# Kernel optimization log

Measured on AMD Instinct MI355X. Metric: run time of the kernel, lower is better.

## Reference

```python
import jax, jax.numpy as jnp
import numpy as np

D_IN, D_K, D_V, BLOCK = 1024, 64, 64, 2048
B, T = 4, 2048

def setup_inputs() -> dict:
    key = jax.random.key(0)
    k0, k1, k2, k3 = jax.random.split(key, 4)
    x = jax.random.normal(k0, (B, T, D_IN), dtype=jnp.float32)
    s = 1.0 / np.sqrt(D_IN)
    Wq = jax.random.normal(k1, (D_IN, D_K), dtype=jnp.float32) * s
    Wk = jax.random.normal(k2, (D_IN, D_K), dtype=jnp.float32) * s
    Wv = jax.random.normal(k3, (D_IN, D_V), dtype=jnp.float32) * s
    return {"x": x, "Wq": Wq, "Wk": Wk, "Wv": Wv}

def reference(x, Wq, Wk, Wv):
    # Q,K,V projections (Linear without bias)
    Q = jnp.einsum('btc,ck->btk', x, Wq)
    K = jnp.einsum('btc,ck->btk', x, Wk)
    V = jnp.einsum('btc,cv->btv', x, Wv)
    Tq = x.shape[1]
    scores = jnp.einsum('bqk,btk->bqt', Q, K)  # [B,T,T]
    causal = jnp.tril(jnp.ones((Tq, Tq), dtype=bool))
    scores = jnp.where(causal, scores, -jnp.inf)
    attn = jax.nn.softmax(scores, axis=-1)
    # NOTE: original divides the AV product by sqrt(d_k) AFTER softmax
    out = jnp.einsum('bqt,btv->bqv', attn, V) / jnp.sqrt(jnp.asarray(K.shape[-1], dtype=x.dtype))
    return out
```

## Files before the change

kernel.cpp:

```cpp
#include <hip/hip_runtime.h>
#include <math.h>

typedef unsigned short u16;
typedef unsigned int uint32;
typedef __attribute__((ext_vector_type(4))) float f32x4;
typedef __attribute__((ext_vector_type(4))) unsigned int u32x4;
typedef __bf16 bf16x8 __attribute__((ext_vector_type(8)));

#define MFMA16(a,b,c) __builtin_amdgcn_mfma_f32_16x16x32_bf16((a),(b),(c),0,0,0)

typedef const __attribute__((address_space(1))) unsigned GU;
typedef __attribute__((address_space(3))) unsigned LU;
__device__ __forceinline__ void gl_lds16(const void* g, void* l) {
    __builtin_amdgcn_global_load_lds((GU*)g, (LU*)l, 16, 0, 0);
}

__device__ __forceinline__ u16 f2b(float f) {
    __bf16 h = (__bf16)f;
    return __builtin_bit_cast(u16, h);
}
__device__ __forceinline__ float b2f(u16 u) {
    unsigned v = (unsigned)u << 16;
    return __builtin_bit_cast(float, v);
}

__device__ __forceinline__ void agload4(f32x4& d, const float* p) {
    asm volatile("global_load_dwordx4 %0, %1, off" : "=&v"(d) : "v"(p) : "memory");
}
__device__ __forceinline__ void dsr(bf16x8& d, uint32 a) {
    u32x4 tmp;
    asm volatile("ds_read_b128 %0, %1" : "=&v"(tmp) : "v"(a) : "memory");
    d = __builtin_bit_cast(bf16x8, tmp);
}
#define WAITVM_I(n) asm volatile("s_waitcnt vmcnt(" #n ")" ::: "memory")
#define WAITVM(n) WAITVM_I(n)

__global__ __launch_bounds__(128) void wtrans_kernel(
    const float* __restrict__ Wq, const float* __restrict__ Wk,
    const float* __restrict__ Wv, u16* __restrict__ Wt2)
{
    const int n = blockIdx.x;
    const float* W = (n < 64) ? Wq : ((n < 128) ? Wk : Wv);
    const int nc = n & 63, cg = n >> 4, r = n & 15;
    const int t = threadIdx.x;
    const int k0 = t * 8;
    const int kstep = k0 >> 6, kh = (k0 >> 5) & 1, kg = (k0 >> 3) & 3;
    u16 hh[8], ll[8];
#pragma unroll
    for (int i = 0; i < 8; ++i) {
        const float a = W[(size_t)(k0 + i) * 64 + nc];
        hh[i] = f2b(a);
        ll[i] = f2b(a - b2f(hh[i]));
    }
    const size_t fi = (size_t)kstep * 48 + (size_t)cg * 4 + (size_t)kh * 2;
    u16* dst = Wt2 + fi * 512 + kg * 128 + r * 8;
    uint4 vh, vl;
    vh.x = (uint)hh[0] | ((uint)hh[1] << 16); vh.y = (uint)hh[2] | ((uint)hh[3] << 16);
    vh.z = (uint)hh[4] | ((uint)hh[5] << 16); vh.w = (uint)hh[6] | ((uint)hh[7] << 16);
    vl.x = (uint)ll[0] | ((uint)ll[1] << 16); vl.y = (uint)ll[2] | ((uint)ll[3] << 16);
    vl.z = (uint)ll[4] | ((uint)ll[5] << 16); vl.w = (uint)ll[6] | ((uint)ll[7] << 16);
    *(uint4*)dst         = vh;
    *(uint4*)(dst + 512) = vl;
}

__global__ __launch_bounds__(512) void proj_kernel(
    const float* __restrict__ x, const u16* __restrict__ Wt2,
    u16* __restrict__ Qhi, u16* __restrict__ Qlo,
    u16* __restrict__ Khi, u16* __restrict__ Klo, u16* __restrict__ Vt)
{
    __shared__ u16 WB[3][48][512];
    __shared__ u16 vs[32][72];

    const int t = threadIdx.x, w = t >> 6, lane = t & 63;
    const int lo = lane & 15, hi = lane >> 4;
    const int mh = w & 1, nt = w >> 1;
    const int row0 = blockIdx.x * 32;

    f32x4 acc[3];
#pragma unroll
    for (int i = 0; i < 3; ++i) acc[i] = (f32x4){0.f, 0.f, 0.f, 0.f};

    const float* xrow = x + (size_t)(row0 + mh * 16 + lo) * 1024 + hi * 8;
    const uint32 ldsbase = (uint32)(size_t)(LU*)(&WB[0][0][0]);

    f32x4 xr[3][4];

    auto stageS = [&](int buf, int s) {
#pragma unroll
        for (int i = 0; i < 6; ++i)
            gl_lds16(Wt2 + ((size_t)s * 48 + w * 6 + i) * 512 + lane * 8,
                     &WB[buf][w * 6 + i][0]);
    };
    auto issueX = [&](f32x4 (&xv)[4], int s) {
#pragma unroll
        for (int kh = 0; kh < 2; ++kh)
#pragma unroll
            for (int j = 0; j < 2; ++j)
                agload4(xv[kh * 2 + j], xrow + s * 64 + kh * 32 + j * 4);
    };
    auto computeS = [&](int buf, const f32x4 (&xv)[4]) {
        bf16x8 wf[12];
        const uint32 bb = ldsbase + (uint32)buf * 49152u
                        + (uint32)(nt * 12) * 1024u + (uint32)lane * 16u;
#pragma unroll
        for (int j = 0; j < 12; ++j)
            dsr(wf[j], bb + (uint32)j * 1024u);
        asm volatile("s_waitcnt lgkmcnt(0)" ::: "memory");
        __builtin_amdgcn_sched_barrier(0);
        __builtin_amdgcn_s_setprio(1);
#pragma unroll
        for (int kh = 0; kh < 2; ++kh) {
            bf16x8 ah, al;
#pragma unroll
            for (int e = 0; e < 4; ++e) {
                { float v = xv[kh * 2][e];     __bf16 hb = (__bf16)v; ah[e] = hb;     al[e] = (__bf16)(v - (float)hb); }
                { float v = xv[kh * 2 + 1][e]; __bf16 hb = (__bf16)v; ah[4 + e] = hb; al[4 + e] = (__bf16)(v - (float)hb); }
            }
#pragma unroll
            for (int i = 0; i < 3; ++i) {
                const bf16x8 wh = wf[i * 4 + kh * 2 + 0];
                const bf16x8 wl = wf[i * 4 + kh * 2 + 1];
                acc[i] = MFMA16(ah, wh, acc[i]);
                acc[i] = MFMA16(ah, wl, acc[i]);
                acc[i] = MFMA16(al, wh, acc[i]);
            }
        }
        __builtin_amdgcn_s_setprio(0);
    };

    stageS(0, 0);
    issueX(xr[0], 0);
    stageS(1, 1);
    issueX(xr[1], 1);

#define PSTEP(S_, N1_)                                                  \
    do {                                                                \
        WAITVM(N1_);                                                    \
        __builtin_amdgcn_sched_barrier(0);                              \
        __builtin_amdgcn_s_barrier();                                   \
        __builtin_amdgcn_sched_barrier(0);                              \
        if ((S_) + 2 <= 15) {                                           \
            stageS(((S_) + 2) % 3, (S_) + 2);                           \
            issueX(xr[((S_) + 2) % 3], (S_) + 2);                       \
        }                                                               \
        computeS((S_) % 3, xr[(S_) % 3]);                               \
    } while (0)

    PSTEP(0, 10);  PSTEP(1, 10);  PSTEP(2, 10);  PSTEP(3, 10);
    PSTEP(4, 10);  PSTEP(5, 10);  PSTEP(6, 10);  PSTEP(7, 10);
    PSTEP(8, 10);  PSTEP(9, 10);  PSTEP(10, 10); PSTEP(11, 10);
    PSTEP(12, 10); PSTEP(13, 10); PSTEP(14, 10); PSTEP(15, 0);
#undef PSTEP

#pragma unroll
    for (int i = 0; i < 3; ++i) {
        const int cg = nt * 3 + i;
#pragma unroll
        for (int r = 0; r < 4; ++r) {
            const float v = acc[i][r];
            const int row = row0 + mh * 16 + hi * 4 + r;
            const u16 h = f2b(v);
            if (cg < 4) {
                Qhi[(size_t)row * 64 + cg * 16 + lo] = h;
                Qlo[(size_t)row * 64 + cg * 16 + lo] = f2b(v - b2f(h));
            } else if (cg < 8) {
                Khi[(size_t)row * 64 + (cg - 4) * 16 + lo] = h;
                Klo[(size_t)row * 64 + (cg - 4) * 16 + lo] = f2b(v - b2f(h));
            } else {
                vs[mh * 16 + hi * 4 + r][(cg - 8) * 16 + lo] = h;
            }
        }
    }
    __syncthreads();
    {
        const int bb = row0 >> 11, tok0 = row0 & 2047;
        const int d = t >> 3, part = t & 7;
        u16 tmp[4];
#pragma unroll
        for (int i = 0; i < 4; ++i) tmp[i] = vs[part * 4 + i][d];
        uint2 v2;
        v2.x = (uint)tmp[0] | ((uint)tmp[1] << 16);
        v2.y = (uint)tmp[2] | ((uint)tmp[3] << 16);
        *(uint2*)(Vt + (size_t)bb * 131072 + (size_t)d * 2048 + tok0 + part * 4) = v2;
    }
}

__global__ __launch_bounds__(512, 2) void attn_kernel(
    const u16* __restrict__ Qhi, const u16* __restrict__ Qlo,
    const u16* __restrict__ Khi, const u16* __restrict__ Klo,
    const u16* __restrict__ Vt, float* __restrict__ out)
{
    __shared__ u16 P[8][16 * 64];
    __shared__ float OA[8][16][64];
    __shared__ float LS[8][16];

    const int pi = blockIdx.x, b = blockIdx.y;
    const int t = threadIdx.x, w = t >> 6, l = t & 63;
    const int lo = l & 15, hi = l >> 4;

    const u16* Qh = Qhi + (size_t)b * 131072;
    const u16* Ql = Qlo + (size_t)b * 131072;
    const u16* Kh = Khi + (size_t)b * 131072;
    const u16* Kl = Klo + (size_t)b * 131072;
    const u16* V  = Vt  + (size_t)b * 131072;

    u16* Pw = P[w];

#pragma unroll 1
    for (int phase = 0; phase < 2; ++phase) {
        const int p = phase ? pi : (127 - pi);
        const int q0 = p * 16;
        const int nt = (p >> 2) + 1;

        bf16x8 aqh[2], aql[2];
#pragma unroll
        for (int s = 0; s < 2; ++s) {
            aqh[s] = *(const bf16x8*)(Qh + (size_t)(q0 + lo) * 64 + s * 32 + hi * 8);
            aql[s] = *(const bf16x8*)(Ql + (size_t)(q0 + lo) * 64 + s * 32 + hi * 8);
        }

        f32x4 acc[4];
        float ls[4];
#pragma unroll
        for (int r = 0; r < 4; ++r) { acc[r] = (f32x4){0.f,0.f,0.f,0.f}; ls[r] = 0.f; }

        bf16x8 kh[4][2], kl[4][2];
        auto loadK = [&](int j0) {
#pragma unroll
            for (int kg = 0; kg < 4; ++kg)
#pragma unroll
                for (int s = 0; s < 2; ++s) {
                    const size_t off = (size_t)(j0 + kg * 16 + lo) * 64 + s * 32 + hi * 8;
                    kh[kg][s] = *(const bf16x8*)(Kh + off);
                    kl[kg][s] = *(const bf16x8*)(Kl + off);
                }
        };

        if (w < nt) loadK(w * 64);
#pragma unroll 1
        for (int j = w; j < nt; j += 8) {
            const int j0 = j * 64;
            bf16x8 bv[4][2];
#pragma unroll
            for (int dg = 0; dg < 4; ++dg)
#pragma unroll
                for (int s = 0; s < 2; ++s)
                    bv[dg][s] = *(const bf16x8*)(V + (size_t)(dg * 16 + lo) * 2048 + j0 + s * 32 + hi * 8);

            f32x4 S[4];
            const f32x4 zf = (f32x4){0.f,0.f,0.f,0.f};
            __builtin_amdgcn_s_setprio(1);
#pragma unroll
            for (int kg = 0; kg < 4; ++kg) {
                f32x4 sv = zf;
                sv = MFMA16(aqh[0], kh[kg][0], sv);
                sv = MFMA16(aqh[1], kh[kg][1], sv);
                sv = MFMA16(aqh[0], kl[kg][0], sv);
                sv = MFMA16(aqh[1], kl[kg][1], sv);
                sv = MFMA16(aql[0], kh[kg][0], sv);
                sv = MFMA16(aql[1], kh[kg][1], sv);
                S[kg] = sv;
            }
            __builtin_amdgcn_s_setprio(0);

            if (j + 8 < nt) loadK((j + 8) * 64);

            const bool dm = (j == nt - 1);
#pragma unroll
            for (int r = 0; r < 4; ++r) {
                const int row = q0 + hi * 4 + r;
                float sv0 = S[0][r], sv1 = S[1][r], sv2 = S[2][r], sv3 = S[3][r];
                if (dm) {
                    sv0 = (j0 +      lo > row) ? -INFINITY : sv0;
                    sv1 = (j0 + 16 + lo > row) ? -INFINITY : sv1;
                    sv2 = (j0 + 32 + lo > row) ? -INFINITY : sv2;
                    sv3 = (j0 + 48 + lo > row) ? -INFINITY : sv3;
                }
                const u16 u0 = f2b(__expf(sv0)), u1 = f2b(__expf(sv1));
                const u16 u2 = f2b(__expf(sv2)), u3 = f2b(__expf(sv3));
                ls[r] += (b2f(u0) + b2f(u1)) + (b2f(u2) + b2f(u3));
                const int rowL = hi * 4 + r;
                const int base = rowL * 64;
                const int sw = rowL & 7;
                Pw[base + (((0 + (lo >> 3)) ^ sw) << 3) + (lo & 7)] = u0;
                Pw[base + (((2 + (lo >> 3)) ^ sw) << 3) + (lo & 7)] = u1;
                Pw[base + (((4 + (lo >> 3)) ^ sw) << 3) + (lo & 7)] = u2;
                Pw[base + (((6 + (lo >> 3)) ^ sw) << 3) + (lo & 7)] = u3;
            }
            const bf16x8 pa0 = *(const bf16x8*)&Pw[lo * 64 + (((hi    ) ^ (lo & 7)) << 3)];
            const bf16x8 pa1 = *(const bf16x8*)&Pw[lo * 64 + (((hi + 4) ^ (lo & 7)) << 3)];
            __builtin_amdgcn_s_setprio(1);
#pragma unroll
            for (int dg = 0; dg < 4; ++dg) {
                acc[dg] = MFMA16(pa0, bv[dg][0], acc[dg]);
                acc[dg] = MFMA16(pa1, bv[dg][1], acc[dg]);
            }
            __builtin_amdgcn_s_setprio(0);
        }

#pragma unroll
        for (int r = 0; r < 4; ++r) {
#pragma unroll
            for (int msk = 8; msk; msk >>= 1) ls[r] += __shfl_xor(ls[r], msk, 64);
        }

#pragma unroll
        for (int r = 0; r < 4; ++r) {
            if (lo == 0) LS[w][hi * 4 + r] = ls[r];
#pragma unroll
            for (int dg = 0; dg < 4; ++dg) OA[w][hi * 4 + r][dg * 16 + lo] = acc[dg][r];
        }
        __syncthreads();

        {
            const int row = t >> 5, c0 = (t & 31) * 2;
            float s0 = 0.f, s1 = 0.f, Lt = 0.f;
#pragma unroll
            for (int wv = 0; wv < 8; ++wv) {
                s0 += OA[wv][row][c0];
                s1 += OA[wv][row][c0 + 1];
                Lt += LS[wv][row];
            }
            const float inv = 0.125f / Lt;
            float2 o = make_float2(s0 * inv, s1 * inv);
            *(float2*)(out + ((size_t)b * 2048 + q0 + row) * 64 + c0) = o;
        }
        __syncthreads();
    }
}

extern "C" void kernel_launch(void* const* d_in, const int* in_sizes, int n_in,
                              void* d_out, int out_size, void* d_ws, size_t ws_size,
                              hipStream_t stream) {
    const float* x  = (const float*)d_in[0];
    const float* Wq = (const float*)d_in[1];
    const float* Wk = (const float*)d_in[2];
    const float* Wv = (const float*)d_in[3];
    float* outp = (float*)d_out;

    u16* Wt2 = (u16*)d_ws;
    u16* Qhi = Wt2 + 393216;
    u16* Qlo = Qhi + 524288;
    u16* Khi = Qlo + 524288;
    u16* Klo = Khi + 524288;
    u16* Vt  = Klo + 524288;

    wtrans_kernel<<<dim3(192), dim3(128), 0, stream>>>(Wq, Wk, Wv, Wt2);
    proj_kernel<<<dim3(256), dim3(512), 0, stream>>>(x, Wt2, Qhi, Qlo, Khi, Klo, Vt);
    attn_kernel<<<dim3(64, 4), dim3(512), 0, stream>>>(Qhi, Qlo, Khi, Klo, Vt, outp);
}
```

Before: 61.51 us.

## Split attention key range across two blocks and add combine kernel; halve projection stage

The attention kernel now launches twice as many blocks. Each block handles half of the key tiles for a query tile and writes unnormalized partial outputs and row sums to workspace. A new combine kernel adds the two halves and applies the normalization. The projection kernel's pipeline stage is halved to 32 columns of K per step, which gives 32 stages with a smaller LDS footprint and fewer registers. The aim is more parallelism and occupancy, paid for with an extra launch and extra global traffic for the partials.

```diff
diff --git a/kernel.cpp b/kernel.cpp
--- a/kernel.cpp
+++ b/kernel.cpp
@@ -68,7 +68,7 @@
     u16* __restrict__ Qhi, u16* __restrict__ Qlo,
     u16* __restrict__ Khi, u16* __restrict__ Klo, u16* __restrict__ Vt)
 {
-    __shared__ u16 WB[3][48][512];
+    __shared__ u16 WB[3][24][512];
     __shared__ u16 vs[32][72];
 
     const int t = threadIdx.x, w = t >> 6, lane = t & 63;
@@ -83,47 +83,44 @@
     const float* xrow = x + (size_t)(row0 + mh * 16 + lo) * 1024 + hi * 8;
     const uint32 ldsbase = (uint32)(size_t)(LU*)(&WB[0][0][0]);
 
-    f32x4 xr[3][4];
+    f32x4 xr[3][2];
 
     auto stageS = [&](int buf, int s) {
 #pragma unroll
-        for (int i = 0; i < 6; ++i)
-            gl_lds16(Wt2 + ((size_t)s * 48 + w * 6 + i) * 512 + lane * 8,
-                     &WB[buf][w * 6 + i][0]);
+        for (int i = 0; i < 3; ++i) {
+            const int j = w * 3 + i;
+            const int cg = j >> 1, hl = j & 1;
+            const size_t fi = (size_t)(s >> 1) * 48 + (size_t)cg * 4 + (size_t)(s & 1) * 2 + hl;
+            gl_lds16(Wt2 + fi * 512 + lane * 8, &WB[buf][j][0]);
+        }
     };
-    auto issueX = [&](f32x4 (&xv)[4], int s) {
-#pragma unroll
-        for (int kh = 0; kh < 2; ++kh)
-#pragma unroll
-            for (int j = 0; j < 2; ++j)
-                agload4(xv[kh * 2 + j], xrow + s * 64 + kh * 32 + j * 4);
+    auto issueX = [&](f32x4 (&xv)[2], int s) {
+        agload4(xv[0], xrow + s * 32);
+        agload4(xv[1], xrow + s * 32 + 4);
     };
-    auto computeS = [&](int buf, const f32x4 (&xv)[4]) {
-        bf16x8 wf[12];
-        const uint32 bb = ldsbase + (uint32)buf * 49152u
-                        + (uint32)(nt * 12) * 1024u + (uint32)lane * 16u;
-#pragma unroll
-        for (int j = 0; j < 12; ++j)
-            dsr(wf[j], bb + (uint32)j * 1024u);
+    auto computeS = [&](int buf, const f32x4 (&xv)[2]) {
+        bf16x8 wf[6];
+        const uint32 bb = ldsbase + (uint32)buf * 24576u + (uint32)lane * 16u;
+#pragma unroll
+        for (int i = 0; i < 3; ++i) {
+            const int cg = nt * 3 + i;
+            dsr(wf[i * 2 + 0], bb + (uint32)(cg * 2 + 0) * 1024u);
+            dsr(wf[i * 2 + 1], bb + (uint32)(cg * 2 + 1) * 1024u);
+        }
         asm volatile("s_waitcnt lgkmcnt(0)" ::: "memory");
         __builtin_amdgcn_sched_barrier(0);
+        bf16x8 ah, al;
+#pragma unroll
+        for (int e = 0; e < 4; ++e) {
+            { float v = xv[0][e]; __bf16 hb = (__bf16)v; ah[e] = hb;     al[e] = (__bf16)(v - (float)hb); }
+            { float v = xv[1][e]; __bf16 hb = (__bf16)v; ah[4 + e] = hb; al[4 + e] = (__bf16)(v - (float)hb); }
+        }
         __builtin_amdgcn_s_setprio(1);
 #pragma unroll
-        for (int kh = 0; kh < 2; ++kh) {
-            bf16x8 ah, al;
-#pragma unroll
-            for (int e = 0; e < 4; ++e) {
-                { float v = xv[kh * 2][e];     __bf16 hb = (__bf16)v; ah[e] = hb;     al[e] = (__bf16)(v - (float)hb); }
-                { float v = xv[kh * 2 + 1][e]; __bf16 hb = (__bf16)v; ah[4 + e] = hb; al[4 + e] = (__bf16)(v - (float)hb); }
-            }
-#pragma unroll
-            for (int i = 0; i < 3; ++i) {
-                const bf16x8 wh = wf[i * 4 + kh * 2 + 0];
-                const bf16x8 wl = wf[i * 4 + kh * 2 + 1];
-                acc[i] = MFMA16(ah, wh, acc[i]);
-                acc[i] = MFMA16(ah, wl, acc[i]);
-                acc[i] = MFMA16(al, wh, acc[i]);
-            }
+        for (int i = 0; i < 3; ++i) {
+            acc[i] = MFMA16(ah, wf[i * 2 + 0], acc[i]);
+            acc[i] = MFMA16(ah, wf[i * 2 + 1], acc[i]);
+            acc[i] = MFMA16(al, wf[i * 2 + 0], acc[i]);
         }
         __builtin_amdgcn_s_setprio(0);
     };
@@ -139,17 +136,21 @@
         __builtin_amdgcn_sched_barrier(0);                              \
         __builtin_amdgcn_s_barrier();                                   \
         __builtin_amdgcn_sched_barrier(0);                              \
-        if ((S_) + 2 <= 15) {                                           \
+        if ((S_) + 2 <= 31) {                                           \
             stageS(((S_) + 2) % 3, (S_) + 2);                           \
             issueX(xr[((S_) + 2) % 3], (S_) + 2);                       \
         }                                                               \
         computeS((S_) % 3, xr[(S_) % 3]);                               \
     } while (0)
 
-    PSTEP(0, 10);  PSTEP(1, 10);  PSTEP(2, 10);  PSTEP(3, 10);
-    PSTEP(4, 10);  PSTEP(5, 10);  PSTEP(6, 10);  PSTEP(7, 10);
-    PSTEP(8, 10);  PSTEP(9, 10);  PSTEP(10, 10); PSTEP(11, 10);
-    PSTEP(12, 10); PSTEP(13, 10); PSTEP(14, 10); PSTEP(15, 0);
+    PSTEP(0, 5);  PSTEP(1, 5);  PSTEP(2, 5);  PSTEP(3, 5);
+    PSTEP(4, 5);  PSTEP(5, 5);  PSTEP(6, 5);  PSTEP(7, 5);
+    PSTEP(8, 5);  PSTEP(9, 5);  PSTEP(10, 5); PSTEP(11, 5);
+    PSTEP(12, 5); PSTEP(13, 5); PSTEP(14, 5); PSTEP(15, 5);
+    PSTEP(16, 5); PSTEP(17, 5); PSTEP(18, 5); PSTEP(19, 5);
+    PSTEP(20, 5); PSTEP(21, 5); PSTEP(22, 5); PSTEP(23, 5);
+    PSTEP(24, 5); PSTEP(25, 5); PSTEP(26, 5); PSTEP(27, 5);
+    PSTEP(28, 5); PSTEP(29, 5); PSTEP(30, 5); PSTEP(31, 0);
 #undef PSTEP
 
 #pragma unroll
@@ -188,15 +189,17 @@
 __global__ __launch_bounds__(512, 2) void attn_kernel(
     const u16* __restrict__ Qhi, const u16* __restrict__ Qlo,
     const u16* __restrict__ Khi, const u16* __restrict__ Klo,
-    const u16* __restrict__ Vt, float* __restrict__ out)
+    const u16* __restrict__ Vt, float* __restrict__ OP, float* __restrict__ LSP)
 {
     __shared__ u16 P[8][16 * 64];
     __shared__ float OA[8][16][64];
     __shared__ float LS[8][16];
 
-    const int pi = blockIdx.x, b = blockIdx.y;
+    const int bx = blockIdx.x, b = blockIdx.y;
+    const int pi = bx >> 1, h = bx & 1;
     const int t = threadIdx.x, w = t >> 6, l = t & 63;
     const int lo = l & 15, hi = l >> 4;
+    const int sw0 = h * 8 + w;
 
     const u16* Qh = Qhi + (size_t)b * 131072;
     const u16* Ql = Qlo + (size_t)b * 131072;
@@ -236,9 +239,9 @@
                 }
         };
 
-        if (w < nt) loadK(w * 64);
+        if (sw0 < nt) loadK(sw0 * 64);
 #pragma unroll 1
-        for (int j = w; j < nt; j += 8) {
+        for (int j = sw0; j < nt; j += 16) {
             const int j0 = j * 64;
             bf16x8 bv[4][2];
 #pragma unroll
@@ -263,7 +266,7 @@
             }
             __builtin_amdgcn_s_setprio(0);
 
-            if (j + 8 < nt) loadK((j + 8) * 64);
+            if (j + 16 < nt) loadK((j + 16) * 64);
 
             const bool dm = (j == nt - 1);
 #pragma unroll
@@ -321,12 +324,28 @@
                 s1 += OA[wv][row][c0 + 1];
                 Lt += LS[wv][row];
             }
-            const float inv = 0.125f / Lt;
-            float2 o = make_float2(s0 * inv, s1 * inv);
-            *(float2*)(out + ((size_t)b * 2048 + q0 + row) * 64 + c0) = o;
+            const size_t gofs = (size_t)h * 524288 + ((size_t)b * 2048 + q0 + row) * 64 + c0;
+            *(float2*)(OP + gofs) = make_float2(s0, s1);
+            if ((t & 31) == 0) LSP[(size_t)h * 8192 + (size_t)b * 2048 + q0 + row] = Lt;
         }
         __syncthreads();
     }
+}
+
+__global__ __launch_bounds__(256) void combine_kernel(
+    const float* __restrict__ OP, const float* __restrict__ LSP, float* __restrict__ out)
+{
+    const int i4 = blockIdx.x * 256 + threadIdx.x;
+    const int row = i4 >> 4;
+    const int c = (i4 & 15) * 4;
+    const float4 a0 = *(const float4*)(OP + ((size_t)row << 6) + c);
+    const float4 a1 = *(const float4*)(OP + 524288 + ((size_t)row << 6) + c);
+    const float Lt = LSP[row] + LSP[8192 + row];
+    const float inv = 0.125f / Lt;
+    float4 o;
+    o.x = (a0.x + a1.x) * inv; o.y = (a0.y + a1.y) * inv;
+    o.z = (a0.z + a1.z) * inv; o.w = (a0.w + a1.w) * inv;
+    *(float4*)(out + ((size_t)row << 6) + c) = o;
 }
 
 extern "C" void kernel_launch(void* const* d_in, const int* in_sizes, int n_in,
@@ -344,8 +363,11 @@
     u16* Khi = Qlo + 524288;
     u16* Klo = Khi + 524288;
     u16* Vt  = Klo + 524288;
+    float* OP  = (float*)(Vt + 524288);
+    float* LSP = OP + 1048576;
 
     wtrans_kernel<<<dim3(192), dim3(128), 0, stream>>>(Wq, Wk, Wv, Wt2);
     proj_kernel<<<dim3(256), dim3(512), 0, stream>>>(x, Wt2, Qhi, Qlo, Khi, Klo, Vt);
-    attn_kernel<<<dim3(64, 4), dim3(512), 0, stream>>>(Qhi, Qlo, Khi, Klo, Vt, outp);
-}
+    attn_kernel<<<dim3(128, 4), dim3(512), 0, stream>>>(Qhi, Qlo, Khi, Klo, Vt, OP, LSP);
+    combine_kernel<<<dim3(512), dim3(256), 0, stream>>>(OP, LSP, outp);
+}
```

New measurement: 76.27 us. 1.24x slower.

## Split projection K-dimension across waves and reduce partial sums via LDS

Applied to the files above, without the earlier changes.

Each wave now handles both 16-row halves but only half of each 64-wide K step, instead of one row half over the full K step. Each wave therefore reads only 6 weight fragments per step instead of 12, so each weight fragment is reused across two row tiles and LDS read traffic drops. The cost is an extra LDS reduction at the end, which adds two barriers. The x global loads are also reorganized per row half.

```diff
diff --git a/kernel.cpp b/kernel.cpp
--- a/kernel.cpp
+++ b/kernel.cpp
@@ -73,56 +73,62 @@
 
     const int t = threadIdx.x, w = t >> 6, lane = t & 63;
     const int lo = lane & 15, hi = lane >> 4;
-    const int mh = w & 1, nt = w >> 1;
+    const int kq = w & 1, nt = w >> 1;
     const int row0 = blockIdx.x * 32;
 
-    f32x4 acc[3];
-#pragma unroll
-    for (int i = 0; i < 3; ++i) acc[i] = (f32x4){0.f, 0.f, 0.f, 0.f};
-
-    const float* xrow = x + (size_t)(row0 + mh * 16 + lo) * 1024 + hi * 8;
+    f32x4 acc[2][3];
+#pragma unroll
+    for (int rh = 0; rh < 2; ++rh)
+#pragma unroll
+        for (int i = 0; i < 3; ++i) acc[rh][i] = (f32x4){0.f, 0.f, 0.f, 0.f};
+
+    const float* xrow0 = x + (size_t)(row0 + lo) * 1024 + kq * 32 + hi * 8;
+    const float* xrow1 = x + (size_t)(row0 + 16 + lo) * 1024 + kq * 32 + hi * 8;
     const uint32 ldsbase = (uint32)(size_t)(LU*)(&WB[0][0][0]);
 
     f32x4 xr[3][4];
 
     auto stageS = [&](int buf, int s) {
 #pragma unroll
-        for (int i = 0; i < 6; ++i)
-            gl_lds16(Wt2 + ((size_t)s * 48 + w * 6 + i) * 512 + lane * 8,
-                     &WB[buf][w * 6 + i][0]);
+        for (int i = 0; i < 3; ++i)
+#pragma unroll
+            for (int hl = 0; hl < 2; ++hl) {
+                const size_t fi = (size_t)s * 48 + (size_t)(nt * 3 + i) * 4
+                                + (size_t)kq * 2 + hl;
+                gl_lds16(Wt2 + fi * 512 + lane * 8, &WB[buf][w * 6 + i * 2 + hl][0]);
+            }
     };
     auto issueX = [&](f32x4 (&xv)[4], int s) {
-#pragma unroll
-        for (int kh = 0; kh < 2; ++kh)
-#pragma unroll
-            for (int j = 0; j < 2; ++j)
-                agload4(xv[kh * 2 + j], xrow + s * 64 + kh * 32 + j * 4);
+        agload4(xv[0], xrow0 + s * 64);
+        agload4(xv[1], xrow0 + s * 64 + 4);
+        agload4(xv[2], xrow1 + s * 64);
+        agload4(xv[3], xrow1 + s * 64 + 4);
     };
     auto computeS = [&](int buf, const f32x4 (&xv)[4]) {
-        bf16x8 wf[12];
+        bf16x8 wf[6];
         const uint32 bb = ldsbase + (uint32)buf * 49152u
-                        + (uint32)(nt * 12) * 1024u + (uint32)lane * 16u;
-#pragma unroll
-        for (int j = 0; j < 12; ++j)
+                        + (uint32)(w * 6) * 1024u + (uint32)lane * 16u;
+#pragma unroll
+        for (int j = 0; j < 6; ++j)
             dsr(wf[j], bb + (uint32)j * 1024u);
         asm volatile("s_waitcnt lgkmcnt(0)" ::: "memory");
         __builtin_amdgcn_sched_barrier(0);
         __builtin_amdgcn_s_setprio(1);
 #pragma unroll
-        for (int kh = 0; kh < 2; ++kh) {
+        for (int rh = 0; rh < 2; ++rh) {
             bf16x8 ah, al;
 #pragma unroll
             for (int e = 0; e < 4; ++e) {
-                { float v = xv[kh * 2][e];     __bf16 hb = (__bf16)v; ah[e] = hb;     al[e] = (__bf16)(v - (float)hb); }
-                { float v = xv[kh * 2 + 1][e]; __bf16 hb = (__bf16)v; ah[4 + e] = hb; al[4 + e] = (__bf16)(v - (float)hb); }
+                { float v = xv[rh * 2][e];     __bf16 hb = (__bf16)v; ah[e] = hb;     al[e] = (__bf16)(v - (float)hb); }
+                { float v = xv[rh * 2 + 1][e]; __bf16 hb = (__bf16)v; ah[4 + e] = hb; al[4 + e] = (__bf16)(v - (float)hb); }
             }
 #pragma unroll
             for (int i = 0; i < 3; ++i) {
-                const bf16x8 wh = wf[i * 4 + kh * 2 + 0];
-                const bf16x8 wl = wf[i * 4 + kh * 2 + 1];
-                acc[i] = MFMA16(ah, wh, acc[i]);
-                acc[i] = MFMA16(ah, wl, acc[i]);
-                acc[i] = MFMA16(al, wh, acc[i]);
+                const bf16x8 wh = wf[i * 2 + 0];
+                const bf16x8 wl = wf[i * 2 + 1];
+                acc[rh][i] = MFMA16(ah, wh, acc[rh][i]);
+                acc[rh][i] = MFMA16(ah, wl, acc[rh][i]);
+                acc[rh][i] = MFMA16(al, wh, acc[rh][i]);
             }
         }
         __builtin_amdgcn_s_setprio(0);
@@ -152,23 +158,44 @@
     PSTEP(12, 10); PSTEP(13, 10); PSTEP(14, 10); PSTEP(15, 0);
 #undef PSTEP
 
-#pragma unroll
-    for (int i = 0; i < 3; ++i) {
-        const int cg = nt * 3 + i;
-#pragma unroll
-        for (int r = 0; r < 4; ++r) {
-            const float v = acc[i][r];
-            const int row = row0 + mh * 16 + hi * 4 + r;
-            const u16 h = f2b(v);
-            if (cg < 4) {
-                Qhi[(size_t)row * 64 + cg * 16 + lo] = h;
-                Qlo[(size_t)row * 64 + cg * 16 + lo] = f2b(v - b2f(h));
-            } else if (cg < 8) {
-                Khi[(size_t)row * 64 + (cg - 4) * 16 + lo] = h;
-                Klo[(size_t)row * 64 + (cg - 4) * 16 + lo] = f2b(v - b2f(h));
-            } else {
-                vs[mh * 16 + hi * 4 + r][(cg - 8) * 16 + lo] = h;
-            }
+    float* PR = (float*)&WB[0][0][0];
+    __syncthreads();
+    if (kq == 1) {
+#pragma unroll
+        for (int rh = 0; rh < 2; ++rh)
+#pragma unroll
+            for (int i = 0; i < 3; ++i)
+                *(f32x4*)&PR[((nt * 6) + rh * 3 + i) * 256 + lane * 4] = acc[rh][i];
+    }
+    __syncthreads();
+    if (kq == 0) {
+#pragma unroll
+        for (int rh = 0; rh < 2; ++rh)
+#pragma unroll
+            for (int i = 0; i < 3; ++i) {
+                const f32x4 o = *(const f32x4*)&PR[((nt * 6) + rh * 3 + i) * 256 + lane * 4];
+                acc[rh][i] += o;
+            }
+#pragma unroll
+        for (int i = 0; i < 3; ++i) {
+            const int cg = nt * 3 + i;
+#pragma unroll
+            for (int rh = 0; rh < 2; ++rh)
+#pragma unroll
+                for (int r = 0; r < 4; ++r) {
+                    const float v = acc[rh][i][r];
+                    const int row = row0 + rh * 16 + hi * 4 + r;
+                    const u16 h = f2b(v);
+                    if (cg < 4) {
+                        Qhi[(size_t)row * 64 + cg * 16 + lo] = h;
+                        Qlo[(size_t)row * 64 + cg * 16 + lo] = f2b(v - b2f(h));
+                    } else if (cg < 8) {
+                        Khi[(size_t)row * 64 + (cg - 4) * 16 + lo] = h;
+                        Klo[(size_t)row * 64 + (cg - 4) * 16 + lo] = f2b(v - b2f(h));
+                    } else {
+                        vs[rh * 16 + hi * 4 + r][(cg - 8) * 16 + lo] = h;
+                    }
+                }
         }
     }
     __syncthreads();
```

New measurement: 63.06 us. +2.5%, slower.
